# Kernel tuning notes

Hardware: AMD Instinct MI355X
Metric: run time of the kernel (lower is better)

Reference implementation:

```python
import jax, jax.numpy as jnp
import numpy as np

ITERS = 3
K = 64
C = 256


def setup_inputs() -> dict:
    key = jax.random.key(0)
    ks = jax.random.split(key, 6)
    N, H, W = 2, 60, 60
    cnn_feature = jax.random.normal(ks[0], (N, C, H, W), dtype=jnp.float32)
    points = jax.random.normal(ks[1], (N, 3, H, W), dtype=jnp.float32)
    # torch Linear params: weight (out, in), bias (out,)
    s1 = 1.0 / np.sqrt(C)
    s2 = 1.0 / np.sqrt(2 * C)
    mlp_w = jax.random.uniform(ks[2], (C, C), jnp.float32, -s1, s1)
    mlp_b = jax.random.uniform(ks[3], (C,), jnp.float32, -s1, s1)
    rnn_w = jax.random.uniform(ks[4], (C, 2 * C), jnp.float32, -s2, s2)
    rnn_b = jax.random.uniform(ks[5], (C,), jnp.float32, -s2, s2)
    return {"cnn_feature": cnn_feature, "points": points, "mlp_w": mlp_w,
            "mlp_b": mlp_b, "rnn_w": rnn_w, "rnn_b": rnn_b}


def reference(cnn_feature, points, mlp_w, mlp_b, rnn_w, rnn_b):
    N, Cc, H, W = cnn_feature.shape
    HW = H * W
    pts = points.reshape(N, 3, HW).transpose(0, 2, 1)  # (N, HW, 3)
    # pairwise Euclidean distances via Gram matrix
    r = jnp.einsum('nid,njd->nij', pts, pts)           # (N, HW, HW)
    sq = jnp.einsum('nid,nid->ni', pts, pts)           # (N, HW)
    D = jnp.sqrt(jnp.maximum(sq[:, :, None] + sq[:, None, :] - 2.0 * r, 0.0))
    _, idx = jax.lax.top_k(-D, K)                      # (N, HW, K) smallest distances

    h = cnn_feature.transpose(0, 2, 3, 1).reshape(N, HW, Cc)  # (N, HW, C)
    bidx = jnp.arange(N)[:, None, None]
    for _ in range(ITERS):
        nb = h[bidx, idx]                              # (N, HW, K, C) gather
        nb = jax.nn.relu(jnp.einsum('nskc,dc->nskd', nb, mlp_w) + mlp_b)
        message = nb.mean(axis=2)                      # (N, HW, C)
        nh = jnp.concatenate([h, message], axis=-1)    # (N, HW, 2C)
        h = jax.nn.relu(jnp.einsum('nsc,dc->nsd', nh, rnn_w) + rnn_b)
    h = h.reshape(N, H, W, Cc).transpose(0, 3, 1, 2)   # (N, C, H, W)
    return jnp.concatenate([cnn_feature, h], axis=1)   # (N, 2C, H, W)
```

## Files before the change

### kernel.cpp

```cpp
#include <hip/hip_runtime.h>
#include <stdint.h>

typedef unsigned int uint;

#define HW 3600
#define NBATCH 2
#define CDIM 256
#define KNN 64
#define M_REAL 7200
#define PADM 7232

using short8  = __attribute__((ext_vector_type(8))) short;
using floatx4 = __attribute__((ext_vector_type(4))) float;

__device__ inline unsigned short f2bf(float f) {
    uint u = __float_as_uint(f);
    uint r = u + 0x7FFFu + ((u >> 16) & 1u);
    return (unsigned short)(r >> 16);
}
__device__ inline float bf2f(unsigned short b) {
    return __uint_as_float(((uint)b) << 16);
}

__device__ inline void hist_select(uint* hist, uint* s_bin, uint* s_want,
                                   int lane, uint want) {
    uint h0 = hist[4 * lane + 0], h1 = hist[4 * lane + 1];
    uint h2 = hist[4 * lane + 2], h3 = hist[4 * lane + 3];
    hist[4 * lane + 0] = 0; hist[4 * lane + 1] = 0;
    hist[4 * lane + 2] = 0; hist[4 * lane + 3] = 0;
    uint c4 = h0 + h1 + h2 + h3;
    uint v = c4;
    #pragma unroll
    for (int off = 1; off < 64; off <<= 1) {
        uint o = __shfl_up(v, off, 64);
        if (lane >= off) v += o;
    }
    uint below = v - c4;
    if (below < want && want <= v) {
        uint b = 4 * lane, c = below;
        if (c + h0 < want) { c += h0; b = 4 * lane + 1;
            if (c + h1 < want) { c += h1; b = 4 * lane + 2;
                if (c + h2 < want) { c += h2; b = 4 * lane + 3; } } }
        *s_bin = b;
        *s_want = want - c;
    }
}

__global__ __launch_bounds__(64) void topk_kernel(const float* __restrict__ points,
                                                  int* __restrict__ idx_out) {
    const int q = blockIdx.x;
    const int n = q / HW;
    const int i = q - n * HW;
    const int lane = threadIdx.x;

    __shared__ uint hist[256];
    __shared__ uint s_bin, s_want, s_cnt;

    const float* __restrict__ px = points + (size_t)n * 3 * HW;
    const float* __restrict__ py = px + HW;
    const float* __restrict__ pz = py + HW;

    hist[4 * lane + 0] = 0; hist[4 * lane + 1] = 0;
    hist[4 * lane + 2] = 0; hist[4 * lane + 3] = 0;
    if (lane == 0) s_cnt = 0;

    const float xi = px[i], yi = py[i], zi = pz[i];
    const float sqi = xi * xi + yi * yi + zi * zi;

    float d2v[57];
    #pragma unroll
    for (int s = 0; s < 57; ++s) {
        int j = (s << 6) + lane;
        float d2 = 1e30f;
        if (j < HW) {
            float xj = px[j], yj = py[j], zj = pz[j];
            d2 = fmaxf(sqi + (xj * xj + yj * yj + zj * zj)
                       - 2.0f * (xi * xj + yi * yj + zi * zj), 0.0f);
        }
        d2v[s] = d2;
    }
    __syncthreads();

    #pragma unroll
    for (int s = 0; s < 57; ++s) {
        uint q16 = (uint)fminf(d2v[s] * 1024.0f, 65535.0f);
        atomicAdd(&hist[q16 >> 8], 1u);
    }
    __syncthreads();
    hist_select(hist, &s_bin, &s_want, lane, KNN);
    __syncthreads();
    const uint qT8 = s_bin;
    const uint want2 = s_want;
    __syncthreads();

    #pragma unroll
    for (int s = 0; s < 57; ++s) {
        uint q16 = (uint)fminf(d2v[s] * 1024.0f, 65535.0f);
        if ((q16 >> 8) == qT8) atomicAdd(&hist[q16 & 255u], 1u);
    }
    __syncthreads();
    hist_select(hist, &s_bin, &s_want, lane, want2);
    __syncthreads();
    const uint qT16 = (qT8 << 8) | s_bin;
    const uint want3 = s_want;

    #pragma unroll
    for (int s = 0; s < 57; ++s) {
        uint q16 = (uint)fminf(d2v[s] * 1024.0f, 65535.0f);
        if (q16 < qT16) {
            uint pos = atomicAdd(&s_cnt, 1u);
            idx_out[(size_t)q * KNN + pos] = (s << 6) + lane;
        }
    }
    unsigned long long used = 0ULL;
    const int base = KNN - (int)want3;
    for (int r = 0; r < (int)want3; ++r) {
        unsigned long long best = ~0ULL;
        #pragma unroll
        for (int s = 0; s < 57; ++s) {
            uint q16 = (uint)fminf(d2v[s] * 1024.0f, 65535.0f);
            if (q16 == qT16 && !((used >> s) & 1ULL)) {
                unsigned long long key =
                    ((unsigned long long)__float_as_uint(d2v[s]) << 32)
                    | (uint)((s << 6) + lane);
                if (key < best) best = key;
            }
        }
        #pragma unroll
        for (int off = 1; off < 64; off <<= 1) {
            unsigned long long o = __shfl_xor(best, off, 64);
            if (o < best) best = o;
        }
        uint jw = (uint)best;
        if (lane == 0) idx_out[(size_t)q * KNN + base + r] = (int)jw;
        if ((int)(jw & 63u) == lane) used |= 1ULL << (jw >> 6);
    }
}

__global__ __launch_bounds__(256) void f32_to_bf16(const float* __restrict__ in,
                                                   unsigned short* __restrict__ out,
                                                   int n) {
    int i = blockIdx.x * 256 + threadIdx.x;
    if (i < n) out[i] = f2bf(in[i]);
}

__global__ __launch_bounds__(256) void init_h(const float* __restrict__ cnn,
                                              unsigned short* __restrict__ NH) {
    __shared__ float tile[32][33];
    const int hw0 = blockIdx.x * 32;
    const int c0 = blockIdx.y * 32;
    const int n = blockIdx.z;
    const int tx = threadIdx.x & 31;
    const int ty = threadIdx.x >> 5;
    const float* __restrict__ src = cnn + (size_t)n * CDIM * HW;
    #pragma unroll
    for (int r = 0; r < 4; ++r) {
        int cc = ty + r * 8;
        int hw = hw0 + tx;
        if (hw < HW) tile[cc][tx] = src[(size_t)(c0 + cc) * HW + hw];
    }
    __syncthreads();
    #pragma unroll
    for (int r = 0; r < 4; ++r) {
        int hh = ty + r * 8;
        int hw = hw0 + hh;
        if (hw < HW) NH[(size_t)(n * HW + hw) * 512 + c0 + tx] = f2bf(tile[tx][hh]);
    }
}

__global__ __launch_bounds__(256) void zero_pads(unsigned short* __restrict__ NHa,
                                                 unsigned short* __restrict__ NHb) {
    int t = blockIdx.x * 256 + threadIdx.x;
    if (t < 32 * 512) {
        NHa[(size_t)M_REAL * 512 + t] = 0;
        NHb[(size_t)M_REAL * 512 + t] = 0;
    }
}

#define LDK 72
__global__ __launch_bounds__(256) void gemm_mfma(
    const unsigned short* __restrict__ A, int lda,
    const unsigned short* __restrict__ W, int ldw,
    const float* __restrict__ bias,
    unsigned short* __restrict__ Cb, float* __restrict__ Cf,
    int ldc, int Kk) {
    __shared__ __align__(16) unsigned short As[64 * LDK];
    __shared__ __align__(16) unsigned short Bs[64 * LDK];
    const int m0 = blockIdx.x * 64;
    const int n0 = blockIdx.y * 64;
    const int tid = threadIdx.x;
    const int lane = tid & 63;
    const int w = tid >> 6;
    const int wm = (w & 1) * 32;
    const int wn = (w >> 1) * 32;
    const int l15 = lane & 15;
    const int qd = lane >> 4;

    floatx4 acc[2][2];
    #pragma unroll
    for (int a = 0; a < 2; ++a)
        #pragma unroll
        for (int b = 0; b < 2; ++b)
            acc[a][b] = (floatx4){0.f, 0.f, 0.f, 0.f};

    const int sr = tid >> 2;
    const int sc = (tid & 3) * 16;

    for (int k0 = 0; k0 < Kk; k0 += 64) {
        const unsigned short* ga = &A[(size_t)(m0 + sr) * lda + k0 + sc];
        const unsigned short* gb = &W[(size_t)(n0 + sr) * ldw + k0 + sc];
        float4 av0 = *(const float4*)(ga);
        float4 av1 = *(const float4*)(ga + 8);
        float4 bv0 = *(const float4*)(gb);
        float4 bv1 = *(const float4*)(gb + 8);
        *(float4*)&As[sr * LDK + sc] = av0;
        *(float4*)&As[sr * LDK + sc + 8] = av1;
        *(float4*)&Bs[sr * LDK + sc] = bv0;
        *(float4*)&Bs[sr * LDK + sc + 8] = bv1;
        __syncthreads();
        #pragma unroll
        for (int ks = 0; ks < 64; ks += 32) {
            short8 a0 = *(const short8*)&As[(wm + l15) * LDK + ks + qd * 8];
            short8 a1 = *(const short8*)&As[(wm + 16 + l15) * LDK + ks + qd * 8];
            short8 b0 = *(const short8*)&Bs[(wn + l15) * LDK + ks + qd * 8];
            short8 b1 = *(const short8*)&Bs[(wn + 16 + l15) * LDK + ks + qd * 8];
            acc[0][0] = __builtin_amdgcn_mfma_f32_16x16x32_bf16(a0, b0, acc[0][0], 0, 0, 0);
            acc[0][1] = __builtin_amdgcn_mfma_f32_16x16x32_bf16(a0, b1, acc[0][1], 0, 0, 0);
            acc[1][0] = __builtin_amdgcn_mfma_f32_16x16x32_bf16(a1, b0, acc[1][0], 0, 0, 0);
            acc[1][1] = __builtin_amdgcn_mfma_f32_16x16x32_bf16(a1, b1, acc[1][1], 0, 0, 0);
        }
        __syncthreads();
    }

    #pragma unroll
    for (int in = 0; in < 2; ++in) {
        int col = n0 + wn + in * 16 + l15;
        float bv = bias[col];
        #pragma unroll
        for (int im = 0; im < 2; ++im) {
            #pragma unroll
            for (int r = 0; r < 4; ++r) {
                int row = m0 + wm + im * 16 + qd * 4 + r;
                float v = fmaxf(acc[im][in][r] + bv, 0.0f);
                if (Cf) Cf[(size_t)row * ldc + col] = v;
                else    Cb[(size_t)row * ldc + col] = f2bf(v);
            }
        }
    }
}

__global__ __launch_bounds__(128) void gather_mean(const unsigned short* __restrict__ T,
                                                   const int* __restrict__ idx,
                                                   unsigned short* __restrict__ NH) {
    const int q = blockIdx.x;
    const int n = q / HW;
    const int t = threadIdx.x;
    __shared__ int nbr[KNN];
    if (t < KNN) nbr[t] = idx[(size_t)q * KNN + t];
    __syncthreads();
    float s0 = 0.0f, s1 = 0.0f;
    #pragma unroll 8
    for (int k = 0; k < KNN; ++k) {
        int r = n * HW + nbr[k];
        uint v = *(const uint*)&T[(size_t)r * CDIM + 2 * t];
        s0 += bf2f((unsigned short)(v & 0xFFFFu));
        s1 += bf2f((unsigned short)(v >> 16));
    }
    uint o = (uint)f2bf(s0 * (1.0f / KNN)) | ((uint)f2bf(s1 * (1.0f / KNN)) << 16);
    *(uint*)&NH[(size_t)q * 512 + CDIM + 2 * t] = o;
}

__global__ __launch_bounds__(256) void copy_cnn(const float* __restrict__ cnn,
                                                float* __restrict__ out) {
    int f = blockIdx.x * 256 + threadIdx.x;
    const int per = CDIM * HW;
    if (f < NBATCH * per) {
        int n = f / per;
        int rem = f - n * per;
        out[(size_t)n * (2 * CDIM * HW) + rem] = cnn[f];
    }
}

__global__ __launch_bounds__(256) void final_out(const float* __restrict__ Hf,
                                                 float* __restrict__ out) {
    __shared__ float tile[32][33];
    const int hw0 = blockIdx.x * 32;
    const int c0 = blockIdx.y * 32;
    const int n = blockIdx.z;
    const int tx = threadIdx.x & 31;
    const int ty = threadIdx.x >> 5;
    #pragma unroll
    for (int r = 0; r < 4; ++r) {
        int hh = ty + r * 8;
        int hw = hw0 + hh;
        if (hw < HW) tile[hh][tx] = Hf[(size_t)(n * HW + hw) * CDIM + c0 + tx];
    }
    __syncthreads();
    #pragma unroll
    for (int r = 0; r < 4; ++r) {
        int cc = ty + r * 8;
        int hw = hw0 + tx;
        if (hw < HW)
            out[(size_t)n * (2 * CDIM * HW) + (size_t)(CDIM + c0 + cc) * HW + hw] =
                tile[tx][cc];
    }
}

extern "C" void kernel_launch(void* const* d_in, const int* in_sizes, int n_in,
                              void* d_out, int out_size, void* d_ws, size_t ws_size,
                              hipStream_t stream) {
    const float* cnn   = (const float*)d_in[0];
    const float* pts   = (const float*)d_in[1];
    const float* mlp_w = (const float*)d_in[2];
    const float* mlp_b = (const float*)d_in[3];
    const float* rnn_w = (const float*)d_in[4];
    const float* rnn_b = (const float*)d_in[5];
    float* out = (float*)d_out;

    unsigned short* NHa    = (unsigned short*)d_ws;
    unsigned short* NHb    = NHa + (size_t)PADM * 512;
    unsigned short* Tb     = NHb + (size_t)PADM * 512;
    unsigned short* mlpw_b = Tb + (size_t)PADM * CDIM;
    unsigned short* rnnw_b = mlpw_b + 65536;
    int*            idx    = (int*)(rnnw_b + 131072);

    f32_to_bf16<<<256, 256, 0, stream>>>(mlp_w, mlpw_b, 65536);
    f32_to_bf16<<<512, 256, 0, stream>>>(rnn_w, rnnw_b, 131072);
    topk_kernel<<<M_REAL, 64, 0, stream>>>(pts, idx);
    init_h<<<dim3(113, 8, NBATCH), 256, 0, stream>>>(cnn, NHa);
    zero_pads<<<64, 256, 0, stream>>>(NHa, NHb);

    unsigned short* cur = NHa;
    unsigned short* nxt = NHb;
    for (int it = 0; it < 3; ++it) {
        gemm_mfma<<<dim3(PADM / 64, CDIM / 64), 256, 0, stream>>>(
            cur, 512, mlpw_b, CDIM, mlp_b, Tb, nullptr, CDIM, CDIM);
        gather_mean<<<M_REAL, 128, 0, stream>>>(Tb, idx, cur);
        if (it < 2)
            gemm_mfma<<<dim3(PADM / 64, CDIM / 64), 256, 0, stream>>>(
                cur, 512, rnnw_b, 512, rnn_b, nxt, nullptr, 512, 512);
        else
            gemm_mfma<<<dim3(PADM / 64, CDIM / 64), 256, 0, stream>>>(
                cur, 512, rnnw_b, 512, rnn_b, nullptr, (float*)nxt, CDIM, 512);
        unsigned short* tmp = cur; cur = nxt; nxt = tmp;
    }

    copy_cnn<<<(NBATCH * CDIM * HW + 255) / 256, 256, 0, stream>>>(cnn, out);
    final_out<<<dim3(113, 8, NBATCH), 256, 0, stream>>>((const float*)cur, out);
}
```

Baseline: 250.1 us.

## Batch top-k queries per block with shared points, vectorize gather, fuse setup kernels

The top-k kernel now runs 8 queries per 512-thread block. It stages the batch's point coordinates in LDS and packs the quantized distances into 16-bit pairs, which cuts register pressure; exact distances are recomputed only for tie candidates. gather_mean uses one wave per query with 16-byte loads and neighbour indices broadcast by shuffle. The weight conversions and pad zeroing are merged into one setup kernel, and the cnn copy to the output is folded into init_h, which removes several launches and a separate pass over the input. Risks include lower occupancy from the large LDS footprint and an added clamp on the gather indices.

Measured after the change: 235.0 us. -6.0%, faster.

```diff
diff --git a/kernel.cpp b/kernel.cpp
--- a/kernel.cpp
+++ b/kernel.cpp
@@ -9,6 +9,7 @@
 #define KNN 64
 #define M_REAL 7200
 #define PADM 7232
+#define QPB 8
 
 using short8  = __attribute__((ext_vector_type(8))) short;
 using floatx4 = __attribute__((ext_vector_type(4))) float;
@@ -22,7 +23,7 @@
     return __uint_as_float(((uint)b) << 16);
 }
 
-__device__ inline void hist_select(uint* hist, uint* s_bin, uint* s_want,
+__device__ inline void wave_select(uint* hist, uint* s_bin, uint* s_want,
                                    int lane, uint want) {
     uint h0 = hist[4 * lane + 0], h1 = hist[4 * lane + 1];
     uint h2 = hist[4 * lane + 2], h3 = hist[4 * lane + 3];
@@ -46,70 +47,73 @@
     }
 }
 
-__global__ __launch_bounds__(64) void topk_kernel(const float* __restrict__ points,
-                                                  int* __restrict__ idx_out) {
-    const int q = blockIdx.x;
-    const int n = q / HW;
+__global__ __launch_bounds__(512) void topk_kernel(const float* __restrict__ points,
+                                                   int* __restrict__ idx_out) {
+    const int wv = threadIdx.x >> 6;
+    const int lane = threadIdx.x & 63;
+    const int q = blockIdx.x * QPB + wv;
+    const int n = (blockIdx.x * QPB) / HW;
     const int i = q - n * HW;
-    const int lane = threadIdx.x;
-
-    __shared__ uint hist[256];
-    __shared__ uint s_bin, s_want, s_cnt;
+
+    __shared__ float sx[HW], sy[HW], sz[HW];
+    __shared__ uint hist[QPB][256];
+    __shared__ uint s_bin[QPB], s_want[QPB], s_cnt[QPB];
 
     const float* __restrict__ px = points + (size_t)n * 3 * HW;
     const float* __restrict__ py = px + HW;
     const float* __restrict__ pz = py + HW;
 
-    hist[4 * lane + 0] = 0; hist[4 * lane + 1] = 0;
-    hist[4 * lane + 2] = 0; hist[4 * lane + 3] = 0;
-    if (lane == 0) s_cnt = 0;
-
-    const float xi = px[i], yi = py[i], zi = pz[i];
+    for (int j = threadIdx.x; j < HW; j += 512) {
+        sx[j] = px[j]; sy[j] = py[j]; sz[j] = pz[j];
+    }
+    hist[wv][4 * lane + 0] = 0; hist[wv][4 * lane + 1] = 0;
+    hist[wv][4 * lane + 2] = 0; hist[wv][4 * lane + 3] = 0;
+    if (lane == 0) s_cnt[wv] = 0;
+    __syncthreads();
+
+    const float xi = sx[i], yi = sy[i], zi = sz[i];
     const float sqi = xi * xi + yi * yi + zi * zi;
 
-    float d2v[57];
+    uint qp[29];
     #pragma unroll
     for (int s = 0; s < 57; ++s) {
         int j = (s << 6) + lane;
-        float d2 = 1e30f;
+        uint q16 = 0xFFFFu;
         if (j < HW) {
-            float xj = px[j], yj = py[j], zj = pz[j];
-            d2 = fmaxf(sqi + (xj * xj + yj * yj + zj * zj)
-                       - 2.0f * (xi * xj + yi * yj + zi * zj), 0.0f);
-        }
-        d2v[s] = d2;
-    }
+            float xj = sx[j], yj = sy[j], zj = sz[j];
+            float d2 = fmaxf(sqi + (xj * xj + yj * yj + zj * zj)
+                             - 2.0f * (xi * xj + yi * yj + zi * zj), 0.0f);
+            q16 = (uint)fminf(d2 * 1024.0f, 65535.0f);
+        }
+        if (s & 1) qp[s >> 1] |= q16 << 16; else qp[s >> 1] = q16;
+    }
+    #define Q16(s) ((qp[(s) >> 1] >> (((s) & 1) << 4)) & 0xFFFFu)
+
+    #pragma unroll
+    for (int s = 0; s < 57; ++s) atomicAdd(&hist[wv][Q16(s) >> 8], 1u);
+    __syncthreads();
+    wave_select(&hist[wv][0], &s_bin[wv], &s_want[wv], lane, KNN);
+    __syncthreads();
+    const uint qT8 = s_bin[wv];
+    const uint want2 = s_want[wv];
     __syncthreads();
 
     #pragma unroll
     for (int s = 0; s < 57; ++s) {
-        uint q16 = (uint)fminf(d2v[s] * 1024.0f, 65535.0f);
-        atomicAdd(&hist[q16 >> 8], 1u);
-    }
-    __syncthreads();
-    hist_select(hist, &s_bin, &s_want, lane, KNN);
-    __syncthreads();
-    const uint qT8 = s_bin;
-    const uint want2 = s_want;
-    __syncthreads();
+        uint k = Q16(s);
+        if ((k >> 8) == qT8) atomicAdd(&hist[wv][k & 255u], 1u);
+    }
+    __syncthreads();
+    wave_select(&hist[wv][0], &s_bin[wv], &s_want[wv], lane, want2);
+    __syncthreads();
+    const uint qT16 = (qT8 << 8) | s_bin[wv];
+    const uint want3 = s_want[wv];
 
     #pragma unroll
     for (int s = 0; s < 57; ++s) {
-        uint q16 = (uint)fminf(d2v[s] * 1024.0f, 65535.0f);
-        if ((q16 >> 8) == qT8) atomicAdd(&hist[q16 & 255u], 1u);
-    }
-    __syncthreads();
-    hist_select(hist, &s_bin, &s_want, lane, want2);
-    __syncthreads();
-    const uint qT16 = (qT8 << 8) | s_bin;
-    const uint want3 = s_want;
-
-    #pragma unroll
-    for (int s = 0; s < 57; ++s) {
-        uint q16 = (uint)fminf(d2v[s] * 1024.0f, 65535.0f);
-        if (q16 < qT16) {
-            uint pos = atomicAdd(&s_cnt, 1u);
-            idx_out[(size_t)q * KNN + pos] = (s << 6) + lane;
+        if (Q16(s) < qT16) {
+            uint pos = atomicAdd(&s_cnt[wv], 1u);
+            if (pos < KNN) idx_out[(size_t)q * KNN + pos] = (s << 6) + lane;
         }
     }
     unsigned long long used = 0ULL;
@@ -118,11 +122,13 @@
         unsigned long long best = ~0ULL;
         #pragma unroll
         for (int s = 0; s < 57; ++s) {
-            uint q16 = (uint)fminf(d2v[s] * 1024.0f, 65535.0f);
-            if (q16 == qT16 && !((used >> s) & 1ULL)) {
+            int j = (s << 6) + lane;
+            if (j < HW && Q16(s) == qT16 && !((used >> s) & 1ULL)) {
+                float xj = sx[j], yj = sy[j], zj = sz[j];
+                float d2 = fmaxf(sqi + (xj * xj + yj * yj + zj * zj)
+                                 - 2.0f * (xi * xj + yi * yj + zi * zj), 0.0f);
                 unsigned long long key =
-                    ((unsigned long long)__float_as_uint(d2v[s]) << 32)
-                    | (uint)((s << 6) + lane);
+                    ((unsigned long long)__float_as_uint(d2) << 32) | (uint)j;
                 if (key < best) best = key;
             }
         }
@@ -135,17 +141,25 @@
         if (lane == 0) idx_out[(size_t)q * KNN + base + r] = (int)jw;
         if ((int)(jw & 63u) == lane) used |= 1ULL << (jw >> 6);
     }
-}
-
-__global__ __launch_bounds__(256) void f32_to_bf16(const float* __restrict__ in,
-                                                   unsigned short* __restrict__ out,
-                                                   int n) {
+    #undef Q16
+}
+
+__global__ __launch_bounds__(256) void setup_kernel(
+    const float* __restrict__ mw, const float* __restrict__ rw,
+    unsigned short* __restrict__ mo, unsigned short* __restrict__ ro,
+    unsigned short* __restrict__ NHa, unsigned short* __restrict__ NHb) {
     int i = blockIdx.x * 256 + threadIdx.x;
-    if (i < n) out[i] = f2bf(in[i]);
+    if (i < 65536) mo[i] = f2bf(mw[i]);
+    ro[i] = f2bf(rw[i]);
+    if (i < 32 * 512) {
+        NHa[(size_t)M_REAL * 512 + i] = 0;
+        NHb[(size_t)M_REAL * 512 + i] = 0;
+    }
 }
 
 __global__ __launch_bounds__(256) void init_h(const float* __restrict__ cnn,
-                                              unsigned short* __restrict__ NH) {
+                                              unsigned short* __restrict__ NH,
+                                              float* __restrict__ out) {
     __shared__ float tile[32][33];
     const int hw0 = blockIdx.x * 32;
     const int c0 = blockIdx.y * 32;
@@ -157,7 +171,11 @@
     for (int r = 0; r < 4; ++r) {
         int cc = ty + r * 8;
         int hw = hw0 + tx;
-        if (hw < HW) tile[cc][tx] = src[(size_t)(c0 + cc) * HW + hw];
+        if (hw < HW) {
+            float v = src[(size_t)(c0 + cc) * HW + hw];
+            tile[cc][tx] = v;
+            out[(size_t)n * (2 * CDIM * HW) + (size_t)(c0 + cc) * HW + hw] = v;
+        }
     }
     __syncthreads();
     #pragma unroll
@@ -165,15 +183,6 @@
         int hh = ty + r * 8;
         int hw = hw0 + hh;
         if (hw < HW) NH[(size_t)(n * HW + hw) * 512 + c0 + tx] = f2bf(tile[tx][hh]);
-    }
-}
-
-__global__ __launch_bounds__(256) void zero_pads(unsigned short* __restrict__ NHa,
-                                                 unsigned short* __restrict__ NHb) {
-    int t = blockIdx.x * 256 + threadIdx.x;
-    if (t < 32 * 512) {
-        NHa[(size_t)M_REAL * 512 + t] = 0;
-        NHb[(size_t)M_REAL * 512 + t] = 0;
     }
 }
 
@@ -249,35 +258,42 @@
     }
 }
 
-__global__ __launch_bounds__(128) void gather_mean(const unsigned short* __restrict__ T,
+__global__ __launch_bounds__(256) void gather_mean(const unsigned short* __restrict__ T,
                                                    const int* __restrict__ idx,
                                                    unsigned short* __restrict__ NH) {
-    const int q = blockIdx.x;
+    const int q = blockIdx.x * 4 + (threadIdx.x >> 6);
+    const int lane = threadIdx.x & 63;
     const int n = q / HW;
-    const int t = threadIdx.x;
-    __shared__ int nbr[KNN];
-    if (t < KNN) nbr[t] = idx[(size_t)q * KNN + t];
-    __syncthreads();
-    float s0 = 0.0f, s1 = 0.0f;
-    #pragma unroll 8
-    for (int k = 0; k < KNN; ++k) {
-        int r = n * HW + nbr[k];
-        uint v = *(const uint*)&T[(size_t)r * CDIM + 2 * t];
-        s0 += bf2f((unsigned short)(v & 0xFFFFu));
-        s1 += bf2f((unsigned short)(v >> 16));
-    }
-    uint o = (uint)f2bf(s0 * (1.0f / KNN)) | ((uint)f2bf(s1 * (1.0f / KNN)) << 16);
-    *(uint*)&NH[(size_t)q * 512 + CDIM + 2 * t] = o;
-}
-
-__global__ __launch_bounds__(256) void copy_cnn(const float* __restrict__ cnn,
-                                                float* __restrict__ out) {
-    int f = blockIdx.x * 256 + threadIdx.x;
-    const int per = CDIM * HW;
-    if (f < NBATCH * per) {
-        int n = f / per;
-        int rem = f - n * per;
-        out[(size_t)n * (2 * CDIM * HW) + rem] = cnn[f];
+    const int half = lane >> 5;
+    const int c8 = (lane & 31) * 8;
+
+    const int nbrL = idx[(size_t)q * KNN + lane];
+    float acc[8] = {0, 0, 0, 0, 0, 0, 0, 0};
+    #pragma unroll 4
+    for (int it = 0; it < 32; ++it) {
+        int k = 2 * it + half;
+        int j = __shfl(nbrL, k, 64);
+        j = min(max(j, 0), HW - 1);
+        int r = n * HW + j;
+        uint4 v = *(const uint4*)&T[(size_t)r * CDIM + c8];
+        acc[0] += bf2f((unsigned short)(v.x & 0xFFFFu));
+        acc[1] += bf2f((unsigned short)(v.x >> 16));
+        acc[2] += bf2f((unsigned short)(v.y & 0xFFFFu));
+        acc[3] += bf2f((unsigned short)(v.y >> 16));
+        acc[4] += bf2f((unsigned short)(v.z & 0xFFFFu));
+        acc[5] += bf2f((unsigned short)(v.z >> 16));
+        acc[6] += bf2f((unsigned short)(v.w & 0xFFFFu));
+        acc[7] += bf2f((unsigned short)(v.w >> 16));
+    }
+    #pragma unroll
+    for (int c = 0; c < 8; ++c) acc[c] += __shfl_xor(acc[c], 32, 64);
+    if (half == 0) {
+        uint4 o;
+        o.x = (uint)f2bf(acc[0] * (1.0f / KNN)) | ((uint)f2bf(acc[1] * (1.0f / KNN)) << 16);
+        o.y = (uint)f2bf(acc[2] * (1.0f / KNN)) | ((uint)f2bf(acc[3] * (1.0f / KNN)) << 16);
+        o.z = (uint)f2bf(acc[4] * (1.0f / KNN)) | ((uint)f2bf(acc[5] * (1.0f / KNN)) << 16);
+        o.w = (uint)f2bf(acc[6] * (1.0f / KNN)) | ((uint)f2bf(acc[7] * (1.0f / KNN)) << 16);
+        *(uint4*)&NH[(size_t)q * 512 + CDIM + c8] = o;
     }
 }
 
@@ -324,18 +340,16 @@
     unsigned short* rnnw_b = mlpw_b + 65536;
     int*            idx    = (int*)(rnnw_b + 131072);
 
-    f32_to_bf16<<<256, 256, 0, stream>>>(mlp_w, mlpw_b, 65536);
-    f32_to_bf16<<<512, 256, 0, stream>>>(rnn_w, rnnw_b, 131072);
-    topk_kernel<<<M_REAL, 64, 0, stream>>>(pts, idx);
-    init_h<<<dim3(113, 8, NBATCH), 256, 0, stream>>>(cnn, NHa);
-    zero_pads<<<64, 256, 0, stream>>>(NHa, NHb);
+    setup_kernel<<<512, 256, 0, stream>>>(mlp_w, rnn_w, mlpw_b, rnnw_b, NHa, NHb);
+    topk_kernel<<<M_REAL / QPB, 512, 0, stream>>>(pts, idx);
+    init_h<<<dim3(113, 8, NBATCH), 256, 0, stream>>>(cnn, NHa, out);
 
     unsigned short* cur = NHa;
     unsigned short* nxt = NHb;
     for (int it = 0; it < 3; ++it) {
         gemm_mfma<<<dim3(PADM / 64, CDIM / 64), 256, 0, stream>>>(
             cur, 512, mlpw_b, CDIM, mlp_b, Tb, nullptr, CDIM, CDIM);
-        gather_mean<<<M_REAL, 128, 0, stream>>>(Tb, idx, cur);
+        gather_mean<<<M_REAL / 4, 256, 0, stream>>>(Tb, idx, cur);
         if (it < 2)
             gemm_mfma<<<dim3(PADM / 64, CDIM / 64), 256, 0, stream>>>(
                 cur, 512, rnnw_b, 512, rnn_b, nxt, nullptr, 512, 512);
@@ -345,6 +359,5 @@
         unsigned short* tmp = cur; cur = nxt; nxt = tmp;
     }
 
-    copy_cnn<<<(NBATCH * CDIM * HW + 255) / 256, 256, 0, stream>>>(cnn, out);
     final_out<<<dim3(113, 8, NBATCH), 256, 0, stream>>>((const float*)cur, out);
 }
```
